# Performance work log

Measured on AMD Instinct MI355X. Metric: run time of the kernel, lower is better.

The kernel has to match this reference:

```python
import jax, jax.numpy as jnp
import numpy as np

BLANK = 0  # blank_index


def lstm_step(x, h, c, W_ih, W_hh, b_ih, b_hh):
    # torch LSTM gate order: i, f, g, o
    gates = x @ W_ih.T + h @ W_hh.T + b_ih + b_hh  # (B, 4H)
    i, f, g, o = jnp.split(gates, 4, axis=-1)
    c2 = jax.nn.sigmoid(f) * c + jax.nn.sigmoid(i) * jnp.tanh(g)
    h2 = jax.nn.sigmoid(o) * jnp.tanh(c2)
    return h2, c2


def greedy_decode(encoder_output, encoded_lengths, embedding, W_ih, W_hh, b_ih, b_hh,
                  W_enc, b_enc, W_pred, b_pred, W_out, b_out, h0, c0):
    # encoder_output: (B, H, T) -> (B, T, H), as in forward()'s transpose(1, 2)
    x = jnp.transpose(encoder_output, (0, 2, 1))
    B, T, H = x.shape

    def step(carry, inputs):
        h, c, last_label = carry          # h,c: (1,B,H); last_label: (B,) int32
        f_t, t = inputs                   # f_t: (B,H) encoder frame, t: scalar int32
        # _pred_step: SOS (zero vector) at t==0, else embed last emitted label
        emb = jnp.where(t == 0, jnp.zeros((B, H), x.dtype), embedding[last_label])
        h1, c1 = lstm_step(emb, h[0], c[0], W_ih, W_hh, b_ih, b_hh)
        # _joint_step: additive joint + relu + output proj, log_softmax (CPU path)
        joint = jax.nn.relu(f_t @ W_enc.T + b_enc + h1 @ W_pred.T + b_pred)
        logp = jax.nn.log_softmax((joint @ W_out.T + b_out).astype(jnp.float32), axis=-1)
        k = jnp.argmax(logp, axis=-1).astype(jnp.int32)  # (B,)
        # blank if past this utterance's length OR argmax is blank
        blank_mask = (t >= encoded_lengths) | (k == BLANK)
        m = blank_mask[:, None]
        # blank entries keep old RNN state and old last_label (original's gather/scatter)
        h_new = jnp.where(m, h[0], h1)[None]
        c_new = jnp.where(m, c[0], c1)[None]
        new_label = jnp.where(blank_mask, last_label, k)
        emitted = jnp.where(blank_mask, BLANK, k)  # blank == nothing emitted this step
        return (h_new, c_new, new_label), emitted

    init = (h0, c0, jnp.full((B,), BLANK, jnp.int32))
    xs = (jnp.transpose(x, (1, 0, 2)), jnp.arange(T, dtype=jnp.int32))
    (hF, cF, _), emitted = jax.lax.scan(step, init, xs)  # emitted: (T, B)
    return emitted.T, hF, cF  # labels (B,T) blank-padded, final (h, c)


def setup_inputs() -> dict:
    key = jax.random.key(0)
    ks = jax.random.split(key, 15)
    B, T, H, V1 = 128, 512, 640, 4097
    s = jnp.float32(0.1)
    return {
        "encoder_output": jax.random.normal(ks[0], (B, H, T), jnp.float32),
        "encoded_lengths": jax.random.randint(ks[1], (B,), 0, T).astype(jnp.int32),
        "embedding": jax.random.normal(ks[2], (V1, H), jnp.float32) * s,
        "W_ih": jax.random.normal(ks[3], (4 * H, H), jnp.float32) * s,
        "W_hh": jax.random.normal(ks[4], (4 * H, H), jnp.float32) * s,
        "b_ih": jax.random.normal(ks[5], (4 * H,), jnp.float32) * s,
        "b_hh": jax.random.normal(ks[6], (4 * H,), jnp.float32) * s,
        "W_enc": jax.random.normal(ks[7], (H, H), jnp.float32) * s,
        "b_enc": jax.random.normal(ks[8], (H,), jnp.float32) * s,
        "W_pred": jax.random.normal(ks[9], (H, H), jnp.float32) * s,
        "b_pred": jax.random.normal(ks[10], (H,), jnp.float32) * s,
        "W_out": jax.random.normal(ks[11], (V1, H), jnp.float32) * s,
        "b_out": jax.random.normal(ks[12], (V1,), jnp.float32) * s,
        "h0": jnp.zeros((1, B, H), jnp.float32),
        "c0": jnp.zeros((1, B, H), jnp.float32),
    }


def reference(encoder_output, encoded_lengths, embedding, W_ih, W_hh, b_ih, b_hh,
              W_enc, b_enc, W_pred, b_pred, W_out, b_out, h0, c0):
    return greedy_decode(encoder_output, encoded_lengths, embedding, W_ih, W_hh,
                         b_ih, b_hh, W_enc, b_enc, W_pred, b_pred, W_out, b_out, h0, c0)
```

## Files before the change

kernel.cpp:

```cpp
#include <hip/hip_runtime.h>
#include <stdint.h>

#define HH 640
#define BB 128
#define TT 512
#define VV 4097
#define G4 2560
#define VP3 4104
#define VE  4112

typedef float f32x4v __attribute__((ext_vector_type(4)));

__device__ __forceinline__ float sigm(float x){ return 1.0f/(1.0f+expf(-x)); }

__device__ __forceinline__ unsigned long long packkey(float f, unsigned v){
    unsigned u = __float_as_uint(f);
    unsigned m = (u & 0x80000000u) ? ~u : (u | 0x80000000u);
    return ((unsigned long long)m << 32) | (unsigned long long)(~v);
}
__device__ __forceinline__ int xcd_tile(int bid, int per){ return (bid & 7)*per + (bid >> 3); }
__device__ __forceinline__ size_t taddr(int k, int b){
    return ((size_t)(k>>2)*BB + b)*4 + (k&3);
}

__global__ __launch_bounds__(256) void k_init3(const float* __restrict__ h0, const float* __restrict__ c0,
                       float* __restrict__ hs0, float* __restrict__ csT,
                       int* __restrict__ label, unsigned long long* __restrict__ slot8){
    int i = blockIdx.x*256 + threadIdx.x;
    if (i < BB*HH){
        int b = i / HH, jj = i % HH;
        size_t o = taddr(jj, b);
        hs0[o] = h0[i]; csT[o] = c0[i];
    }
    if (i < BB) label[i] = 0;
    if (i < 8*BB) slot8[i] = 0ULL;
}

__global__ __launch_bounds__(256) void k_tr_gate(const float* __restrict__ W, float* __restrict__ WT){
    int idx = blockIdx.x*256 + threadIdx.x;
    if (idx >= G4*160) return;
    int row = idx / 160, kq = idx % 160;
    int g = row / HH, jj = row % HH;
    float4 f = *reinterpret_cast<const float4*>(W + (size_t)row*HH + kq*4);
    WT[(size_t)(kq*4+0)*G4 + jj*4+g] = f.x;
    WT[(size_t)(kq*4+1)*G4 + jj*4+g] = f.y;
    WT[(size_t)(kq*4+2)*G4 + jj*4+g] = f.z;
    WT[(size_t)(kq*4+3)*G4 + jj*4+g] = f.w;
}
__global__ __launch_bounds__(256) void k_tr640(const float* __restrict__ W, float* __restrict__ WT){
    int idx = blockIdx.x*256 + threadIdx.x;
    if (idx >= HH*160) return;
    int n = idx / 160, kq = idx % 160;
    float4 f = *reinterpret_cast<const float4*>(W + (size_t)n*HH + kq*4);
    WT[(size_t)(kq*4+0)*HH + n] = f.x;
    WT[(size_t)(kq*4+1)*HH + n] = f.y;
    WT[(size_t)(kq*4+2)*HH + n] = f.z;
    WT[(size_t)(kq*4+3)*HH + n] = f.w;
}
__global__ __launch_bounds__(256) void k_tr_wout3(const float* __restrict__ W, float* __restrict__ WT){
    int idx = blockIdx.x*256 + threadIdx.x;
    if (idx >= VP3*160) return;
    int v = idx / 160, kq = idx % 160;
    float4 f = make_float4(0.f,0.f,0.f,0.f);
    if (v < VV) f = *reinterpret_cast<const float4*>(W + (size_t)v*HH + kq*4);
    WT[(size_t)(kq*4+0)*VP3 + v] = f.x;
    WT[(size_t)(kq*4+1)*VP3 + v] = f.y;
    WT[(size_t)(kq*4+2)*VP3 + v] = f.z;
    WT[(size_t)(kq*4+3)*VP3 + v] = f.w;
}
__global__ __launch_bounds__(256) void k_boutpad3(const float* __restrict__ b_out, float* __restrict__ boutP){
    int v = blockIdx.x*256 + threadIdx.x;
    if (v < VP3) boutP[v] = (v < VV) ? b_out[v] : -1e30f;
}
__global__ __launch_bounds__(256) void k_tr_embT(const float* __restrict__ emb, float* __restrict__ embT){
    int idx = blockIdx.x*256 + threadIdx.x;
    if (idx >= 160*VE) return;
    int kq = idx / VE, v = idx % VE;
    float4 f = make_float4(0.f,0.f,0.f,0.f);
    if (v < VV) f = *reinterpret_cast<const float4*>(emb + (size_t)v*HH + kq*4);
    embT[(size_t)(kq*4+0)*VE + v] = f.x;
    embT[(size_t)(kq*4+1)*VE + v] = f.y;
    embT[(size_t)(kq*4+2)*VE + v] = f.z;
    embT[(size_t)(kq*4+3)*VE + v] = f.w;
}

__global__ __launch_bounds__(256) void k_embproj3(const float* __restrict__ embT,
                          const float* __restrict__ WihT,
                          const float* __restrict__ b_ih, const float* __restrict__ b_hh,
                          float* __restrict__ embproj){
    __shared__ float lwv[HH*16];
    int vt = blockIdx.x / 160, ut = blockIdx.x % 160;
    for (int i=threadIdx.x; i<HH*16; i+=256)
        lwv[i] = WihT[(size_t)(i>>4)*G4 + ut*16 + (i&15)];
    float bias[16];
    #pragma unroll
    for (int u=0;u<16;++u){
        int gu = ut*16+u, jj = gu>>2, g = gu&3;
        bias[u] = b_ih[g*HH+jj] + b_hh[g*HH+jj];
    }
    __syncthreads();
    int v = vt*256 + threadIdx.x;
    float acc[16];
    #pragma unroll
    for (int u=0;u<16;++u) acc[u]=0.f;
    if (v < VV){
        #pragma unroll 2
        for (int k=0;k<HH;++k){
            float e = embT[(size_t)k*VE + v];
            const f32x4v* wr = reinterpret_cast<const f32x4v*>(&lwv[k*16]);
            #pragma unroll
            for (int g=0; g<4; ++g){
                f32x4v w = wr[g];
                #pragma unroll
                for (int ee=0; ee<4; ++ee) acc[g*4+ee] = fmaf(w[ee], e, acc[g*4+ee]);
            }
        }
    }
    if (v <= VV){
        #pragma unroll
        for (int q=0;q<4;++q){
            float4 st = make_float4(acc[q*4+0]+bias[q*4+0], acc[q*4+1]+bias[q*4+1],
                                    acc[q*4+2]+bias[q*4+2], acc[q*4+3]+bias[q*4+3]);
            *reinterpret_cast<float4*>(embproj + (size_t)v*G4 + ut*16 + q*4) = st;
        }
    }
}

__global__ __launch_bounds__(128) void k_encprojT2(const float* __restrict__ x,
                          const float* __restrict__ WencT, const float* __restrict__ b_enc,
                          float* __restrict__ encprojT){
    int tile = (blockIdx.x & 7)*2560 + (blockIdx.x >> 3);
    int b   = tile / 160;
    int rem = tile % 160;
    int tt  = rem / 5;
    int nt2 = rem % 5;
    int n = nt2*128 + threadIdx.x;
    float acc[16];
    #pragma unroll
    for (int i=0;i<16;i++) acc[i]=0.f;
    const float* xb = x + (size_t)b*HH*TT + tt*16;
    #pragma unroll 4
    for (int k=0;k<HH;++k){
        float wv = WencT[(size_t)k*HH + n];
        const float4* xp = reinterpret_cast<const float4*>(xb + (size_t)k*TT);
        float4 x0=xp[0], x1=xp[1], x2=xp[2], x3=xp[3];
        acc[0]=fmaf(x0.x,wv,acc[0]);  acc[1]=fmaf(x0.y,wv,acc[1]);
        acc[2]=fmaf(x0.z,wv,acc[2]);  acc[3]=fmaf(x0.w,wv,acc[3]);
        acc[4]=fmaf(x1.x,wv,acc[4]);  acc[5]=fmaf(x1.y,wv,acc[5]);
        acc[6]=fmaf(x1.z,wv,acc[6]);  acc[7]=fmaf(x1.w,wv,acc[7]);
        acc[8]=fmaf(x2.x,wv,acc[8]);  acc[9]=fmaf(x2.y,wv,acc[9]);
        acc[10]=fmaf(x2.z,wv,acc[10]); acc[11]=fmaf(x2.w,wv,acc[11]);
        acc[12]=fmaf(x3.x,wv,acc[12]); acc[13]=fmaf(x3.y,wv,acc[13]);
        acc[14]=fmaf(x3.z,wv,acc[14]); acc[15]=fmaf(x3.w,wv,acc[15]);
    }
    float be = b_enc[n];
    #pragma unroll
    for (int ti=0; ti<16; ++ti)
        encprojT[((size_t)(tt*16+ti)*HH + n)*BB + b] = acc[ti] + be;
}


__global__ __launch_bounds__(512) void kA(
    const float* __restrict__ WhhT, const float* __restrict__ embproj,
    const int* __restrict__ lens,
    const float* __restrict__ hsrT, float* __restrict__ hswT,
    const float* __restrict__ h1rT, float* __restrict__ h1wT,
    float* __restrict__ csT, float* __restrict__ c1T,
    int* __restrict__ label, const unsigned long long* __restrict__ slot8,
    float* __restrict__ out_emit, int t)
{
    __shared__ float lw[HH*16];
    __shared__ float red[3*16*128];
    const int bid = xcd_tile(blockIdx.x, 20);
    const int tid = threadIdx.x;
    const int b = tid & 127, kh = tid >> 7;
    const int u0 = bid*16;

    for (int i=tid; i<HH*16; i+=512)
        lw[i] = WhhT[(size_t)(i>>4)*G4 + u0 + (i&15)];

    bool mask; int sel=0, kprev=0;
    if (t==0){ mask=true; sel=0; }
    else{
        unsigned long long key = slot8[b];
        #pragma unroll
        for (int q=1;q<8;++q){ unsigned long long o=slot8[q*128+b]; if(o>key)key=o; }
        int k = (int)(~(unsigned)key);
        int lab = label[b];
        mask = ((t-1) >= lens[b]) || (k==0);
        kprev = k; sel = mask ? lab : k;
    }
    __syncthreads();

    const float4* hp = reinterpret_cast<const float4*>(mask ? hsrT : h1rT);
    float a1[16];
    #pragma unroll
    for (int u=0;u<16;++u) a1[u]=0.f;
    const int k0 = kh*40;
    #pragma unroll 2
    for (int k4=k0; k4<k0+40; ++k4){
        float4 hv = hp[(size_t)k4*BB + b];
        #pragma unroll
        for (int q=0;q<4;++q){
            float h = (q==0)?hv.x:(q==1)?hv.y:(q==2)?hv.z:hv.w;
            const f32x4v* wr = reinterpret_cast<const f32x4v*>(&lw[(k4*4+q)*16]);
            #pragma unroll
            for (int g=0; g<4; ++g){
                f32x4v w = wr[g];
                #pragma unroll
                for (int ee=0; ee<4; ++ee) a1[g*4+ee] = fmaf(w[ee], h, a1[g*4+ee]);
            }
        }
    }
    if (kh > 0){
        #pragma unroll
        for (int u=0;u<16;++u) red[((kh-1)*16+u)*128 + b] = a1[u];
    }
    __syncthreads();
    if (kh == 0){
        int erow = (t==0) ? VV : sel;
        const float4* eb = reinterpret_cast<const float4*>(embproj + (size_t)erow*G4 + u0);
        const size_t g4 = (size_t)bid*BB + b;
        float4 ce4 = mask ? reinterpret_cast<const float4*>(csT)[g4]
                          : reinterpret_cast<const float4*>(c1T)[g4];
        float4 he4 = mask ? reinterpret_cast<const float4*>(hsrT)[g4]
                          : reinterpret_cast<const float4*>(h1rT)[g4];
        float cn[4], hn[4];
        const float* cep = &ce4.x;
        #pragma unroll
        for (int jl=0; jl<4; ++jl){
            float4 e = eb[jl];
            float gi = a1[jl*4+0] + red[(jl*4+0)*128+b] + red[(16+jl*4+0)*128+b] + red[(32+jl*4+0)*128+b] + e.x;
            float gf = a1[jl*4+1] + red[(jl*4+1)*128+b] + red[(16+jl*4+1)*128+b] + red[(32+jl*4+1)*128+b] + e.y;
            float gg = a1[jl*4+2] + red[(jl*4+2)*128+b] + red[(16+jl*4+2)*128+b] + red[(32+jl*4+2)*128+b] + e.z;
            float go = a1[jl*4+3] + red[(jl*4+3)*128+b] + red[(16+jl*4+3)*128+b] + red[(32+jl*4+3)*128+b] + e.w;
            float ce = cep[jl];
            float cv = sigm(gf)*ce + sigm(gi)*tanhf(gg);
            cn[jl] = cv;
            hn[jl] = sigm(go)*tanhf(cv);
        }
        reinterpret_cast<float4*>(csT)[g4]  = ce4;
        reinterpret_cast<float4*>(c1T)[g4]  = make_float4(cn[0],cn[1],cn[2],cn[3]);
        reinterpret_cast<float4*>(hswT)[g4] = he4;
        reinterpret_cast<float4*>(h1wT)[g4] = make_float4(hn[0],hn[1],hn[2],hn[3]);
        if (bid == 0){
            if (t > 0) out_emit[(size_t)b*TT + (t-1)] = mask ? 0.f : (float)kprev;
            label[b] = sel;
        }
    }
}

__global__ __launch_bounds__(512) void kB(
    const float* __restrict__ WpredT, const float* __restrict__ encprojT,
    const float* __restrict__ b_pred, const float* __restrict__ h1T,
    float* __restrict__ jointT, unsigned long long* __restrict__ slot8, int t)
{
    __shared__ float lw[HH*4];
    __shared__ float red[3*4*128];
    const int bid = xcd_tile(blockIdx.x, 20);
    const int tid = threadIdx.x;
    const int b = tid & 127, kh = tid >> 7;
    const int n0 = bid*4;
    for (int i=tid; i<HH*4; i+=512)
        lw[i] = WpredT[(size_t)(i>>2)*HH + n0 + (i&3)];
    if (bid == 0 && kh == 3){
        #pragma unroll
        for (int q=0;q<8;++q) slot8[q*128 + b] = 0ULL;
    }
    __syncthreads();
    const float4* hp = reinterpret_cast<const float4*>(h1T);
    float a[4] = {0.f,0.f,0.f,0.f};
    const int k0 = kh*40;
    #pragma unroll 2
    for (int k4=k0; k4<k0+40; ++k4){
        float4 hv = hp[(size_t)k4*BB + b];
        #pragma unroll
        for (int q=0;q<4;++q){
            float h = (q==0)?hv.x:(q==1)?hv.y:(q==2)?hv.z:hv.w;
            f32x4v w = *reinterpret_cast<const f32x4v*>(&lw[(k4*4+q)*4]);
            #pragma unroll
            for (int ee=0; ee<4; ++ee) a[ee] = fmaf(w[ee], h, a[ee]);
        }
    }
    if (kh > 0){
        #pragma unroll
        for (int u=0;u<4;++u) red[((kh-1)*4+u)*128 + b] = a[u];
    }
    __syncthreads();
    if (kh == 0){
        float jn[4];
        #pragma unroll
        for (int u=0;u<4;++u){
            float s = a[u] + red[u*128+b] + red[(4+u)*128+b] + red[(8+u)*128+b]
                    + b_pred[n0+u] + encprojT[((size_t)t*HH + n0+u)*BB + b];
            jn[u] = fmaxf(s, 0.f);
        }
        reinterpret_cast<float4*>(jointT)[(size_t)bid*BB + b] =
            make_float4(jn[0],jn[1],jn[2],jn[3]);
    }
}

__global__ __launch_bounds__(512) void kC(
    const float* __restrict__ WoutT3, const float* __restrict__ boutP3,
    const float* __restrict__ jointT, unsigned long long* __restrict__ slot8)
{
    __shared__ float lw[HH*20];
    __shared__ float red[3*19*128];
    const int bid = xcd_tile(blockIdx.x, 27);
    const int tid = threadIdx.x;
    const int b = tid & 127, kh = tid >> 7;
    const int v0 = bid*19;
    for (int i=tid; i<HH*19; i+=512){
        int k = i/19, u = i - k*19;
        lw[k*20 + u] = WoutT3[(size_t)k*VP3 + v0 + u];
    }
    __syncthreads();
    const float4* jp = reinterpret_cast<const float4*>(jointT);
    float a[19];
    #pragma unroll
    for (int u=0;u<19;++u) a[u]=0.f;
    const int k0 = kh*40;
    #pragma unroll 2
    for (int k4=k0; k4<k0+40; ++k4){
        float4 jv = jp[(size_t)k4*BB + b];
        #pragma unroll
        for (int q=0;q<4;++q){
            float h = (q==0)?jv.x:(q==1)?jv.y:(q==2)?jv.z:jv.w;
            const f32x4v* wr = reinterpret_cast<const f32x4v*>(&lw[(k4*4+q)*20]);
            #pragma unroll
            for (int g=0; g<4; ++g){
                f32x4v w = wr[g];
                #pragma unroll
                for (int ee=0; ee<4; ++ee) a[g*4+ee] = fmaf(w[ee], h, a[g*4+ee]);
            }
            f32x4v w4 = wr[4];
            a[16] = fmaf(w4[0], h, a[16]);
            a[17] = fmaf(w4[1], h, a[17]);
            a[18] = fmaf(w4[2], h, a[18]);
        }
    }
    if (kh > 0){
        #pragma unroll
        for (int u=0;u<19;++u) red[((kh-1)*19+u)*128 + b] = a[u];
    }
    __syncthreads();
    if (kh == 0){
        unsigned long long key = 0ULL;
        #pragma unroll
        for (int u=0;u<19;++u){
            float s = a[u] + red[u*128+b] + red[(19+u)*128+b] + red[(38+u)*128+b] + boutP3[v0+u];
            unsigned long long kk = packkey(s, (unsigned)(v0+u));
            if (kk > key) key = kk;
        }
        atomicMax(&slot8[(bid&7)*128 + b], key);
    }
}

__global__ __launch_bounds__(256) void kFin(const int* __restrict__ lens,
                        const unsigned long long* __restrict__ slot8,
                        const float* __restrict__ hsT, const float* __restrict__ h1T,
                        const float* __restrict__ csT, const float* __restrict__ c1T,
                        float* __restrict__ dout)
{
    int i = blockIdx.x*256 + threadIdx.x;
    if (i >= BB*HH) return;
    int b = i / HH, jj = i % HH;
    unsigned long long key = slot8[b];
    #pragma unroll
    for (int q=1;q<8;++q){ unsigned long long o=slot8[q*128+b]; if(o>key)key=o; }
    int k = (int)(~(unsigned)key);
    bool m = ((TT-1) >= lens[b]) || (k == 0);
    size_t o = taddr(jj, b);
    dout[BB*TT + i]         = m ? hsT[o] : h1T[o];
    dout[BB*TT + BB*HH + i] = m ? csT[o] : c1T[o];
    if (i < BB){
        unsigned long long key2 = slot8[i];
        #pragma unroll
        for (int q=1;q<8;++q){ unsigned long long o2=slot8[q*128+i]; if(o2>key2)key2=o2; }
        int k2 = (int)(~(unsigned)key2);
        bool mm = ((TT-1) >= lens[i]) || (k2 == 0);
        dout[(size_t)i*TT + (TT-1)] = mm ? 0.0f : (float)k2;
    }
}

__global__ __launch_bounds__(256) void k_init(const float* __restrict__ h0, const float* __restrict__ c0,
                       float* __restrict__ hs0, float* __restrict__ cs,
                       int* __restrict__ label, unsigned long long* __restrict__ slot){
    int i = blockIdx.x*256 + threadIdx.x;
    if (i < BB*HH){ hs0[i] = h0[i]; cs[i] = c0[i]; }
    if (i < BB){ label[i] = 0; slot[i] = 0ULL; }
}

__global__ __launch_bounds__(256) void k_p1o(
    const float* __restrict__ Whh, const float* __restrict__ Wih,
    const float* __restrict__ embedding,
    const float* __restrict__ b_ih, const float* __restrict__ b_hh,
    const int* __restrict__ lens,
    const float* __restrict__ hs_r, float* __restrict__ hs_w,
    const float* __restrict__ h1_r, float* __restrict__ h1_w,
    float* c_state, float* c1, int* label,
    const unsigned long long* __restrict__ slot,
    float* __restrict__ out_emit, int t)
{
    int tile = (blockIdx.x & 7)*20 + (blockIdx.x >> 3);
    int jt = tile >> 4, bg = tile & 15;
    int lane = threadIdx.x & 63, w = threadIdx.x >> 6;
    int j = (jt<<6) + lane, b0 = bg<<3;

    bool mask[8]; int kprev[8]; int sel[8];
    #pragma unroll
    for (int bi=0; bi<8; ++bi){
        int b = b0+bi;
        if (t == 0){ mask[bi]=true; sel[bi]=0; kprev[bi]=0; }
        else {
            unsigned long long key = slot[b];
            int k = (int)(~(unsigned)key);
            int lab = label[b];
            bool m = ((t-1) >= lens[b]) || (k == 0);
            mask[bi]=m; kprev[bi]=k; sel[bi] = m ? lab : k;
        }
    }
    float acc[8];
    #pragma unroll
    for (int i=0;i<8;i++) acc[i]=0.f;
    const float* wrow  = Whh + (size_t)(w*HH + j)*HH;
    const float* wrow2 = Wih + (size_t)(w*HH + j)*HH;
    for (int kc=0; kc<HH; kc+=16){
        float wv[16], wv2[16];
        #pragma unroll
        for (int q=0;q<4;q++){
            float4 f = *reinterpret_cast<const float4*>(wrow + kc + q*4);
            wv[q*4+0]=f.x; wv[q*4+1]=f.y; wv[q*4+2]=f.z; wv[q*4+3]=f.w;
            float4 f2 = *reinterpret_cast<const float4*>(wrow2 + kc + q*4);
            wv2[q*4+0]=f2.x; wv2[q*4+1]=f2.y; wv2[q*4+2]=f2.z; wv2[q*4+3]=f2.w;
        }
        #pragma unroll
        for (int bi=0; bi<8; ++bi){
            int b = b0+bi;
            const float* hp0 = hs_r + (size_t)b*HH + kc;
            const float* hp1 = h1_r + (size_t)b*HH + kc;
            float a = acc[bi];
            if (mask[bi]){
                #pragma unroll
                for (int k=0;k<16;k++) a = fmaf(hp0[k], wv[k], a);
            } else {
                #pragma unroll
                for (int k=0;k<16;k++) a = fmaf(hp1[k], wv[k], a);
            }
            if (t > 0){
                const float* ep = embedding + (size_t)sel[bi]*HH + kc;
                #pragma unroll
                for (int k=0;k<16;k++) a = fmaf(ep[k], wv2[k], a);
            }
            acc[bi] = a;
        }
    }
    __shared__ float xch[8][4][64];
    #pragma unroll
    for (int bi=0; bi<8; ++bi)
        xch[bi][w][lane] = acc[bi] + b_ih[w*HH + j] + b_hh[w*HH + j];
    __syncthreads();
    #pragma unroll
    for (int r=0; r<2; ++r){
        int bi = (w<<1) + r;
        int b  = b0 + bi;
        size_t o = (size_t)b*HH + j;
        float gi = xch[bi][0][lane], gf = xch[bi][1][lane];
        float gg = xch[bi][2][lane], go = xch[bi][3][lane];
        float ce = mask[bi] ? c_state[o] : c1[o];
        float c2 = sigm(gf)*ce + sigm(gi)*tanhf(gg);
        float h2 = sigm(go)*tanhf(c2);
        float he = mask[bi] ? hs_r[o] : h1_r[o];
        c_state[o] = ce; c1[o] = c2; hs_w[o] = he; h1_w[o] = h2;
    }
    if (jt == 0 && t > 0 && threadIdx.x < 8){
        int bi = threadIdx.x; int b = b0 + bi;
        out_emit[(size_t)b*TT + (t-1)] = mask[bi] ? 0.0f : (float)kprev[bi];
        label[b] = sel[bi];
    }
}

__global__ __launch_bounds__(128) void k_p2o(
    const float* __restrict__ Wpred, const float* __restrict__ Wenc,
    const float* __restrict__ x, const float* __restrict__ b_enc,
    const float* __restrict__ b_pred, const float* __restrict__ h1,
    float* __restrict__ joint, unsigned long long* __restrict__ slot, int t)
{
    int tile = (blockIdx.x & 7)*20 + (blockIdx.x >> 3);
    int nt = tile / 32, bg = tile % 32;
    int lane = threadIdx.x & 63, w = threadIdx.x >> 6;
    int n = nt*128 + w*64 + lane, b0 = bg*4;
    float acc[4] = {0.f,0.f,0.f,0.f};
    const float* wr  = Wpred + (size_t)n*HH;
    const float* wr2 = Wenc  + (size_t)n*HH;
    for (int kc=0; kc<HH; kc+=16){
        float wv[16], wv2[16];
        #pragma unroll
        for (int q=0;q<4;q++){
            float4 f = *reinterpret_cast<const float4*>(wr + kc + q*4);
            wv[q*4+0]=f.x; wv[q*4+1]=f.y; wv[q*4+2]=f.z; wv[q*4+3]=f.w;
            float4 f2 = *reinterpret_cast<const float4*>(wr2 + kc + q*4);
            wv2[q*4+0]=f2.x; wv2[q*4+1]=f2.y; wv2[q*4+2]=f2.z; wv2[q*4+3]=f2.w;
        }
        #pragma unroll
        for (int bi=0; bi<4; ++bi){
            int b = b0+bi;
            const float* hp = h1 + (size_t)b*HH + kc;
            float a = acc[bi];
            #pragma unroll
            for (int k=0;k<16;k++) a = fmaf(hp[k], wv[k], a);
            const float* xp = x + (size_t)b*HH*TT + (size_t)kc*TT + t;
            #pragma unroll
            for (int k=0;k<16;k++) a = fmaf(xp[(size_t)k*TT], wv2[k], a);
            acc[bi] = a;
        }
    }
    #pragma unroll
    for (int bi=0; bi<4; ++bi){
        int b = b0+bi;
        joint[(size_t)b*HH + n] = fmaxf(acc[bi] + b_pred[n] + b_enc[n], 0.0f);
    }
    if (tile == 0) slot[threadIdx.x] = 0ULL;
}

__global__ __launch_bounds__(256) void k_p3o(
    const float* __restrict__ Wout, const float* __restrict__ b_out,
    const float* __restrict__ joint, unsigned long long* __restrict__ slot)
{
    int tile = (blockIdx.x & 7)*34 + (blockIdx.x >> 3);
    int vt = tile >> 4, bg = tile & 15;
    int lane = threadIdx.x & 63, w = threadIdx.x >> 6;
    int v = vt*256 + w*64 + lane;
    bool valid = v < VV;
    int vv = valid ? v : (VV-1);
    int b0 = bg*8;
    float acc[8];
    #pragma unroll
    for (int i=0;i<8;i++) acc[i]=0.f;
    const float* wr = Wout + (size_t)vv*HH;
    for (int kc=0; kc<HH; kc+=16){
        float wv[16];
        #pragma unroll
        for (int q=0;q<4;q++){
            float4 f = *reinterpret_cast<const float4*>(wr + kc + q*4);
            wv[q*4+0]=f.x; wv[q*4+1]=f.y; wv[q*4+2]=f.z; wv[q*4+3]=f.w;
        }
        #pragma unroll
        for (int bi=0; bi<8; ++bi){
            int b = b0+bi;
            const float* jp = joint + (size_t)b*HH + kc;
            float a = acc[bi];
            #pragma unroll
            for (int k=0;k<16;k++) a = fmaf(jp[k], wv[k], a);
            acc[bi] = a;
        }
    }
    float bofl = b_out[vv];
    __shared__ unsigned long long redo[4][8];
    #pragma unroll
    for (int bi=0; bi<8; ++bi){
        unsigned long long key = valid ? packkey(acc[bi] + bofl, (unsigned)v) : 0ULL;
        #pragma unroll
        for (int off=32; off>0; off>>=1){
            unsigned long long o = __shfl_xor(key, off, 64);
            if (o > key) key = o;
        }
        if (lane == 0) redo[w][bi] = key;
    }
    __syncthreads();
    if (threadIdx.x < 8){
        int bi = threadIdx.x;
        unsigned long long m = redo[0][bi];
        #pragma unroll
        for (int q=1;q<4;q++) if (redo[q][bi] > m) m = redo[q][bi];
        atomicMax(&slot[b0+bi], m);
    }
}

__global__ __launch_bounds__(256) void k_finalo(const int* __restrict__ lens,
                        const unsigned long long* __restrict__ slot,
                        const float* __restrict__ hs_r, const float* __restrict__ h1_r,
                        const float* __restrict__ cs,  const float* __restrict__ c1,
                        float* __restrict__ dout)
{
    int i = blockIdx.x*256 + threadIdx.x;
    if (i >= BB*HH) return;
    int b = i / HH;
    unsigned long long key = slot[b];
    int k = (int)(~(unsigned)key);
    bool m = ((TT-1) >= lens[b]) || (k == 0);
    dout[BB*TT + i]         = m ? hs_r[i] : h1_r[i];
    dout[BB*TT + BB*HH + i] = m ? cs[i]   : c1[i];
    if (i < BB){
        unsigned long long key2 = slot[i];
        int k2 = (int)(~(unsigned)key2);
        bool mm = ((TT-1) >= lens[i]) || (k2 == 0);
        dout[(size_t)i*TT + (TT-1)] = mm ? 0.0f : (float)k2;
    }
}

extern "C" void kernel_launch(void* const* d_in, const int* in_sizes, int n_in,
                              void* d_out, int out_size, void* d_ws, size_t ws_size,
                              hipStream_t stream)
{
    const float* x     = (const float*)d_in[0];
    const int*   lens  = (const int*)  d_in[1];
    const float* emb   = (const float*)d_in[2];
    const float* Wih   = (const float*)d_in[3];
    const float* Whh   = (const float*)d_in[4];
    const float* bih   = (const float*)d_in[5];
    const float* bhh   = (const float*)d_in[6];
    const float* Wenc  = (const float*)d_in[7];
    const float* benc  = (const float*)d_in[8];
    const float* Wpred = (const float*)d_in[9];
    const float* bpred = (const float*)d_in[10];
    const float* Wout  = (const float*)d_in[11];
    const float* bout  = (const float*)d_in[12];
    const float* h0    = (const float*)d_in[13];
    const float* c0    = (const float*)d_in[14];
    float* out = (float*)d_out;
    (void)in_sizes; (void)n_in; (void)out_size;

    char* ws = (char*)d_ws;
    size_t off = 0;
    auto alloc = [&](size_t bytes) -> void* {
        void* p = ws + off; off += (bytes + 255) & ~(size_t)255; return p;
    };
    auto aligned = [](size_t bytes){ return (bytes + 255) & ~(size_t)255; };

    const size_t BH = (size_t)BB*HH*sizeof(float);
    float* hs0  = (float*)alloc(BH);
    float* hs1  = (float*)alloc(BH);
    float* h1b0 = (float*)alloc(BH);
    float* h1b1 = (float*)alloc(BH);
    float* cs   = (float*)alloc(BH);
    float* c1   = (float*)alloc(BH);
    float* joint= (float*)alloc(BH);
    int* label  = (int*)alloc(BB*sizeof(int));
    unsigned long long* slot8 = (unsigned long long*)alloc(8*BB*sizeof(unsigned long long));

    size_t need = off
        + aligned((size_t)HH*G4*sizeof(float))
        + aligned((size_t)HH*G4*sizeof(float))
        + aligned((size_t)HH*HH*sizeof(float))
        + aligned((size_t)HH*HH*sizeof(float))
        + aligned((size_t)HH*VP3*sizeof(float))
        + aligned((size_t)VP3*sizeof(float))
        + aligned((size_t)HH*VE*sizeof(float))
        + aligned((size_t)(VV+1)*G4*sizeof(float))
        + aligned((size_t)TT*BB*HH*sizeof(float));

    if (ws_size >= need){
        float* WhhT   = (float*)alloc((size_t)HH*G4*sizeof(float));
        float* WihT   = (float*)alloc((size_t)HH*G4*sizeof(float));
        float* WpredT = (float*)alloc((size_t)HH*HH*sizeof(float));
        float* WencT  = (float*)alloc((size_t)HH*HH*sizeof(float));
        float* WoutT3 = (float*)alloc((size_t)HH*VP3*sizeof(float));
        float* boutP3 = (float*)alloc((size_t)VP3*sizeof(float));
        float* embT   = (float*)alloc((size_t)HH*VE*sizeof(float));
        float* embproj= (float*)alloc((size_t)(VV+1)*G4*sizeof(float));
        float* encprojT=(float*)alloc((size_t)TT*BB*HH*sizeof(float));

        k_init3<<<(BB*HH+255)/256, 256, 0, stream>>>(h0, c0, hs0, cs, label, slot8);
        k_tr_gate<<<(G4*160+255)/256, 256, 0, stream>>>(Whh, WhhT);
        k_tr_gate<<<(G4*160+255)/256, 256, 0, stream>>>(Wih, WihT);
        k_tr640 <<<(HH*160+255)/256, 256, 0, stream>>>(Wpred, WpredT);
        k_tr640 <<<(HH*160+255)/256, 256, 0, stream>>>(Wenc,  WencT);
        k_tr_wout3<<<(VP3*160+255)/256, 256, 0, stream>>>(Wout, WoutT3);
        k_boutpad3<<<(VP3+255)/256, 256, 0, stream>>>(bout, boutP3);
        k_tr_embT<<<(160*VE+255)/256, 256, 0, stream>>>(emb, embT);
        k_embproj3<<<17*160, 256, 0, stream>>>(embT, WihT, bih, bhh, embproj);
        k_encprojT2<<<20480, 128, 0, stream>>>(x, WencT, benc, encprojT);

        float* hsbuf[2] = {hs0, hs1};
        float* h1buf[2] = {h1b0, h1b1};
        for (int t = 0; t < TT; ++t){
            const float* hsr = hsbuf[t & 1];
            float*       hsw = hsbuf[(t+1) & 1];
            const float* h1r = h1buf[(t+1) & 1];
            float*       h1w = h1buf[t & 1];
            kA<<<160, 512, 0, stream>>>(WhhT, embproj, lens, hsr, hsw, h1r, h1w,
                                        cs, c1, label, slot8, out, t);
            kB<<<160, 512, 0, stream>>>(WpredT, encprojT, bpred, h1w, joint, slot8, t);
            kC<<<216, 512, 0, stream>>>(WoutT3, boutP3, joint, slot8);
        }
        kFin<<<(BB*HH+255)/256, 256, 0, stream>>>(lens, slot8, hsbuf[0], h1buf[1], cs, c1, out);
        return;
    }

    unsigned long long* slot = slot8;
    k_init<<<(BB*HH+255)/256, 256, 0, stream>>>(h0, c0, hs0, cs, label, slot);
    float* hsbuf[2] = {hs0, hs1};
    float* h1buf[2] = {h1b0, h1b1};
    for (int t = 0; t < TT; ++t){
        const float* hsr = hsbuf[t & 1];
        float*       hsw = hsbuf[(t+1) & 1];
        const float* h1r = h1buf[(t+1) & 1];
        float*       h1w = h1buf[t & 1];
        k_p1o<<<160, 256, 0, stream>>>(Whh, Wih, emb, bih, bhh, lens,
                                       hsr, hsw, h1r, h1w, cs, c1, label, slot, out, t);
        k_p2o<<<160, 128, 0, stream>>>(Wpred, Wenc, x, benc, bpred, h1w, joint, slot, t);
        k_p3o<<<272, 256, 0, stream>>>(Wout, bout, joint, slot);
    }
    k_finalo<<<(BB*HH+255)/256, 256, 0, stream>>>(lens, slot, hsbuf[0], h1buf[1], cs, c1, out);
}
```

Baseline: 33.09 ms.

## Replace per-step kernel launches with persistent cooperative kernel using per-XCD barriers

Replaces the three kernel launches per timestep (1536 launches in total) with a single persistent cooperative kernel of 256 blocks. Each XCD owns 16 batch rows and synchronises through atomic spin barriers in global memory. The kernel also fuses the W_hh and W_pred matvecs into one concatenated weight matrix, computing the gate pre-activations for the next step together with the joint projection, and uses new k4-interleaved weight layouts. The aim is to remove launch overhead and inter-kernel gaps. The cost is reliance on co-residency, hardware XCD id reads, volatile memory traffic and spin-wait timeouts, which adds correctness and deadlock risk.

```diff
diff --git a/kernel.cpp b/kernel.cpp
--- a/kernel.cpp
+++ b/kernel.cpp
@@ -6,8 +6,11 @@
 #define TT 512
 #define VV 4097
 #define G4 2560
-#define VP3 4104
-#define VE  4112
+#define VE 4112
+#define XS 10240
+#define XG 40960
+#define NC2 3200
+#define NC3 4096
 
 typedef float f32x4v __attribute__((ext_vector_type(4)));
 
@@ -18,22 +21,26 @@
     unsigned m = (u & 0x80000000u) ? ~u : (u | 0x80000000u);
     return ((unsigned long long)m << 32) | (unsigned long long)(~v);
 }
-__device__ __forceinline__ int xcd_tile(int bid, int per){ return (bid & 7)*per + (bid >> 3); }
-__device__ __forceinline__ size_t taddr(int k, int b){
-    return ((size_t)(k>>2)*BB + b)*4 + (k&3);
-}
-
-__global__ __launch_bounds__(256) void k_init3(const float* __restrict__ h0, const float* __restrict__ c0,
-                       float* __restrict__ hs0, float* __restrict__ csT,
-                       int* __restrict__ label, unsigned long long* __restrict__ slot8){
+
+__device__ __forceinline__ float vld(const float* p){ return *(const volatile float*)p; }
+__device__ __forceinline__ void  vst(float* p, float v){ *(volatile float*)p = v; }
+__device__ __forceinline__ int   vldi(const int* p){ return *(const volatile int*)p; }
+__device__ __forceinline__ void  vsti(int* p, int v){ *(volatile int*)p = v; }
+
+__global__ __launch_bounds__(256) void k_init4(const float* __restrict__ h0, const float* __restrict__ c0,
+                       float* __restrict__ hcm, float* __restrict__ cs,
+                       int* __restrict__ labelP, unsigned long long* __restrict__ slot,
+                       int* __restrict__ ctrl){
     int i = blockIdx.x*256 + threadIdx.x;
     if (i < BB*HH){
         int b = i / HH, jj = i % HH;
-        size_t o = taddr(jj, b);
-        hs0[o] = h0[i]; csT[o] = c0[i];
-    }
-    if (i < BB) label[i] = 0;
-    if (i < 8*BB) slot8[i] = 0ULL;
+        int x = b >> 4, bl = b & 15;
+        size_t o = (size_t)x*XS + jj*16 + bl;
+        hcm[o] = h0[i]; cs[o] = c0[i];
+    }
+    if (i < BB) slot[i] = 0ULL;
+    if (i < 8*32) labelP[i] = 0;
+    if (i < 2048) ctrl[i] = 0;
 }
 
 __global__ __launch_bounds__(256) void k_tr_gate(const float* __restrict__ W, float* __restrict__ WT){
@@ -57,21 +64,6 @@
     WT[(size_t)(kq*4+2)*HH + n] = f.z;
     WT[(size_t)(kq*4+3)*HH + n] = f.w;
 }
-__global__ __launch_bounds__(256) void k_tr_wout3(const float* __restrict__ W, float* __restrict__ WT){
-    int idx = blockIdx.x*256 + threadIdx.x;
-    if (idx >= VP3*160) return;
-    int v = idx / 160, kq = idx % 160;
-    float4 f = make_float4(0.f,0.f,0.f,0.f);
-    if (v < VV) f = *reinterpret_cast<const float4*>(W + (size_t)v*HH + kq*4);
-    WT[(size_t)(kq*4+0)*VP3 + v] = f.x;
-    WT[(size_t)(kq*4+1)*VP3 + v] = f.y;
-    WT[(size_t)(kq*4+2)*VP3 + v] = f.z;
-    WT[(size_t)(kq*4+3)*VP3 + v] = f.w;
-}
-__global__ __launch_bounds__(256) void k_boutpad3(const float* __restrict__ b_out, float* __restrict__ boutP){
-    int v = blockIdx.x*256 + threadIdx.x;
-    if (v < VP3) boutP[v] = (v < VV) ? b_out[v] : -1e30f;
-}
 __global__ __launch_bounds__(256) void k_tr_embT(const float* __restrict__ emb, float* __restrict__ embT){
     int idx = blockIdx.x*256 + threadIdx.x;
     if (idx >= 160*VE) return;
@@ -82,6 +74,30 @@
     embT[(size_t)(kq*4+1)*VE + v] = f.y;
     embT[(size_t)(kq*4+2)*VE + v] = f.z;
     embT[(size_t)(kq*4+3)*VE + v] = f.w;
+}
+__global__ __launch_bounds__(256) void k_tr_WJ(const float* __restrict__ Whh, const float* __restrict__ Wpred,
+                        float* __restrict__ WJ){
+    int idx = blockIdx.x*256 + threadIdx.x;
+    if (idx >= NC2*160) return;
+    int u = idx / 160, k4 = idx % 160;
+    float4 f;
+    if (u < G4){
+        int jj = u >> 2, g = u & 3;
+        f = *reinterpret_cast<const float4*>(Whh + (size_t)(g*HH+jj)*HH + k4*4);
+    } else {
+        int n = u - G4;
+        f = *reinterpret_cast<const float4*>(Wpred + (size_t)n*HH + k4*4);
+    }
+    float* d = WJ + ((size_t)k4*NC2 + u)*4;
+    d[0]=f.x; d[1]=f.y; d[2]=f.z; d[3]=f.w;
+}
+__global__ __launch_bounds__(256) void k_tr_woutk4(const float* __restrict__ Wout, float* __restrict__ WK){
+    int idx = blockIdx.x*256 + threadIdx.x;
+    if (idx >= NC3*160) return;
+    int v = idx / 160, k4 = idx % 160;
+    float4 f = *reinterpret_cast<const float4*>(Wout + (size_t)v*HH + k4*4);
+    float* d = WK + ((size_t)k4*NC3 + v)*4;
+    d[0]=f.x; d[1]=f.y; d[2]=f.z; d[3]=f.w;
 }
 
 __global__ __launch_bounds__(256) void k_embproj3(const float* __restrict__ embT,
@@ -159,224 +175,280 @@
         encprojT[((size_t)(tt*16+ti)*HH + n)*BB + b] = acc[ti] + be;
 }
 
-
-__global__ __launch_bounds__(512) void kA(
-    const float* __restrict__ WhhT, const float* __restrict__ embproj,
-    const int* __restrict__ lens,
-    const float* __restrict__ hsrT, float* __restrict__ hswT,
-    const float* __restrict__ h1rT, float* __restrict__ h1wT,
-    float* __restrict__ csT, float* __restrict__ c1T,
-    int* __restrict__ label, const unsigned long long* __restrict__ slot8,
-    float* __restrict__ out_emit, int t)
+__global__ __launch_bounds__(512) void k_gcm0(const float* __restrict__ WJ, const float* __restrict__ h0,
+                       float* __restrict__ gcm){
+    __shared__ float stage[XS];
+    __shared__ float red[3*128*16];
+    int x = blockIdx.x / 20, rr = blockIdx.x % 20;
+    int tid = threadIdx.x;
+    for (int i=tid; i<XS; i+=512)
+        stage[i] = h0[(size_t)(x*16 + (i&15))*HH + (i>>4)];
+    __syncthreads();
+    const int lane = tid & 127, kq = tid >> 7;
+    const int u = rr*128 + lane;
+    float acc[16];
+    #pragma unroll
+    for (int j=0;j<16;++j) acc[j]=0.f;
+    const float4* wp = reinterpret_cast<const float4*>(WJ) + (size_t)(kq*40)*NC2 + u;
+    for (int it=0; it<40; ++it){
+        float4 wj = *wp; wp += NC2;
+        const int kb = (kq*40 + it)*4;
+        #pragma unroll
+        for (int ks=0; ks<4; ++ks){
+            float wk = (ks==0)?wj.x:(ks==1)?wj.y:(ks==2)?wj.z:wj.w;
+            const float4* hp4 = reinterpret_cast<const float4*>(&stage[(kb+ks)*16]);
+            float4 h0v=hp4[0], h1v=hp4[1], h2v=hp4[2], h3v=hp4[3];
+            acc[0]=fmaf(wk,h0v.x,acc[0]);  acc[1]=fmaf(wk,h0v.y,acc[1]);
+            acc[2]=fmaf(wk,h0v.z,acc[2]);  acc[3]=fmaf(wk,h0v.w,acc[3]);
+            acc[4]=fmaf(wk,h1v.x,acc[4]);  acc[5]=fmaf(wk,h1v.y,acc[5]);
+            acc[6]=fmaf(wk,h1v.z,acc[6]);  acc[7]=fmaf(wk,h1v.w,acc[7]);
+            acc[8]=fmaf(wk,h2v.x,acc[8]);  acc[9]=fmaf(wk,h2v.y,acc[9]);
+            acc[10]=fmaf(wk,h2v.z,acc[10]); acc[11]=fmaf(wk,h2v.w,acc[11]);
+            acc[12]=fmaf(wk,h3v.x,acc[12]); acc[13]=fmaf(wk,h3v.y,acc[13]);
+            acc[14]=fmaf(wk,h3v.z,acc[14]); acc[15]=fmaf(wk,h3v.w,acc[15]);
+        }
+    }
+    if (kq > 0){
+        #pragma unroll
+        for (int j=0;j<16;++j) red[(kq-1)*2048 + lane*16 + j] = acc[j];
+    }
+    __syncthreads();
+    if (kq == 0){
+        #pragma unroll
+        for (int j=0;j<16;++j) acc[j] += red[lane*16+j] + red[2048+lane*16+j] + red[4096+lane*16+j];
+        int jj = u >> 2, g = u & 3;
+        #pragma unroll
+        for (int bl=0; bl<16; ++bl)
+            gcm[(size_t)x*XG + (jj*16+bl)*4 + g] = acc[bl];
+    }
+}
+
+__global__ __launch_bounds__(512,1) void k_run(
+    const float* __restrict__ WJ, const float* __restrict__ WoutK4,
+    const float* __restrict__ WoutRaw, const float* __restrict__ b_pred,
+    const float* __restrict__ b_out, const float* __restrict__ embproj,
+    const float* __restrict__ encprojT, const int* __restrict__ lens,
+    float* hcm, float* h1s, float* cs, float* c1,
+    float* gcm, float* gnew, float* jointA,
+    unsigned long long* slot, int* labelP, int* ctrl,
+    float* dout, int guard)
 {
-    __shared__ float lw[HH*16];
-    __shared__ float red[3*16*128];
-    const int bid = xcd_tile(blockIdx.x, 20);
+    __shared__ float stage[XS];
+    __shared__ float red[3*128*16];
+    __shared__ unsigned long long keys[128*16];
+    __shared__ float padf[2048];
     const int tid = threadIdx.x;
-    const int b = tid & 127, kh = tid >> 7;
-    const int u0 = bid*16;
-
-    for (int i=tid; i<HH*16; i+=512)
-        lw[i] = WhhT[(size_t)(i>>4)*G4 + u0 + (i&15)];
-
-    bool mask; int sel=0, kprev=0;
-    if (t==0){ mask=true; sel=0; }
-    else{
-        unsigned long long key = slot8[b];
-        #pragma unroll
-        for (int q=1;q<8;++q){ unsigned long long o=slot8[q*128+b]; if(o>key)key=o; }
-        int k = (int)(~(unsigned)key);
-        int lab = label[b];
-        mask = ((t-1) >= lens[b]) || (k==0);
-        kprev = k; sel = mask ? lab : k;
+    if (guard){ padf[tid & 2047] = (float)guard; stage[0] += padf[1]; }
+
+    int xcd = __builtin_amdgcn_s_getreg(63508) & 7;
+
+    __shared__ int s_r, s_R;
+    if (tid == 0){
+        s_r = (int)__hip_atomic_fetch_add((unsigned*)&ctrl[xcd], 1u, __ATOMIC_RELAXED, __HIP_MEMORY_SCOPE_AGENT);
+        __hip_atomic_fetch_add((unsigned*)&ctrl[16], 1u, __ATOMIC_RELAXED, __HIP_MEMORY_SCOPE_AGENT);
+        long spin = 0;
+        while (__hip_atomic_load((unsigned*)&ctrl[16], __ATOMIC_RELAXED, __HIP_MEMORY_SCOPE_AGENT) < 256u
+               && spin < 400000000L){ __builtin_amdgcn_s_sleep(1); ++spin; }
+        s_R = (int)__hip_atomic_load((unsigned*)&ctrl[xcd], __ATOMIC_RELAXED, __HIP_MEMORY_SCOPE_AGENT);
     }
     __syncthreads();
-
-    const float4* hp = reinterpret_cast<const float4*>(mask ? hsrT : h1rT);
-    float a1[16];
-    #pragma unroll
-    for (int u=0;u<16;++u) a1[u]=0.f;
-    const int k0 = kh*40;
-    #pragma unroll 2
-    for (int k4=k0; k4<k0+40; ++k4){
-        float4 hv = hp[(size_t)k4*BB + b];
-        #pragma unroll
-        for (int q=0;q<4;++q){
-            float h = (q==0)?hv.x:(q==1)?hv.y:(q==2)?hv.z:hv.w;
-            const f32x4v* wr = reinterpret_cast<const f32x4v*>(&lw[(k4*4+q)*16]);
+    const int r = s_r;
+    const int R = s_R;
+    unsigned* bcp = (unsigned*)&ctrl[32 + xcd*32];
+    const int b0 = xcd*16;
+
+    float* hcmX = hcm + (size_t)xcd*XS;
+    float* h1X  = h1s + (size_t)xcd*XS;
+    float* csX  = cs  + (size_t)xcd*XS;
+    float* c1X  = c1  + (size_t)xcd*XS;
+    float* gcmX = gcm + (size_t)xcd*XG;
+    float* gnewX= gnew+ (size_t)xcd*XG;
+    float* jX   = jointA + (size_t)xcd*XS;
+    int* labX   = labelP + xcd*32;
+
+    unsigned ph = 0;
+    #define LBAR() do { \
+        asm volatile("s_waitcnt vmcnt(0) lgkmcnt(0)" ::: "memory"); \
+        __syncthreads(); \
+        ++ph; \
+        if (tid == 0){ \
+            __hip_atomic_fetch_add(bcp, 1u, __ATOMIC_RELAXED, __HIP_MEMORY_SCOPE_AGENT); \
+            long spin = 0; unsigned tgt = ph * (unsigned)R; \
+            while (__hip_atomic_load(bcp, __ATOMIC_RELAXED, __HIP_MEMORY_SCOPE_AGENT) < tgt \
+                   && spin < 400000000L){ __builtin_amdgcn_s_sleep(1); ++spin; } \
+        } \
+        __syncthreads(); \
+        asm volatile("" ::: "memory"); \
+    } while(0)
+
+    for (int t = 0; t < TT; ++t){
+        for (int u = r*512 + tid; u < XS; u += R*512){
+            int jj = u >> 4, bl = u & 15, b = b0 + bl;
+            bool mask; int sel = 0, kprev = 0;
+            if (t == 0){ mask = true; sel = 0; }
+            else {
+                unsigned long long key = __hip_atomic_load(&slot[b], __ATOMIC_RELAXED, __HIP_MEMORY_SCOPE_AGENT);
+                int k = (int)(~(unsigned)key);
+                int lab = vldi(labX + bl);
+                mask = ((t-1) >= lens[b]) || (k == 0);
+                kprev = k; sel = mask ? lab : k;
+            }
+            size_t go = (size_t)u*4;
+            const float* gs = (mask ? gcmX : gnewX) + go;
+            float ghx = vld(gs+0), ghy = vld(gs+1), ghz = vld(gs+2), ghw = vld(gs+3);
+            if (!mask){ float* gd = gcmX + go; vst(gd+0,ghx); vst(gd+1,ghy); vst(gd+2,ghz); vst(gd+3,ghw); }
+            int erow = (t == 0) ? VV : sel;
+            float4 e = reinterpret_cast<const float4*>(embproj)[(size_t)erow*640 + jj];
+            float gi = ghx+e.x, gf = ghy+e.y, gg = ghz+e.z, goo = ghw+e.w;
+            float ce = mask ? vld(csX+u) : vld(c1X+u);
+            float cv = sigm(gf)*ce + sigm(gi)*tanhf(gg);
+            float h2 = sigm(goo)*tanhf(cv);
+            float he = mask ? vld(hcmX+u) : vld(h1X+u);
+            vst(csX+u, ce); vst(c1X+u, cv); vst(hcmX+u, he); vst(h1X+u, h2);
+            if (jj == 0){
+                if (t > 0) dout[(size_t)b*TT + (t-1)] = mask ? 0.f : (float)kprev;
+                vsti(labX + bl, sel);
+            }
+        }
+        LBAR();
+
+        for (int i = tid; i < XS; i += 512) stage[i] = vld(h1X + i);
+        if (r == R-1 && tid < 16)
+            __hip_atomic_store(&slot[b0+tid], 0ULL, __ATOMIC_RELAXED, __HIP_MEMORY_SCOPE_AGENT);
+        __syncthreads();
+        for (int w = r; w < 25; w += R){
+            const int lane = tid & 127, kq = tid >> 7;
+            const int u = w*128 + lane;
+            float acc[16];
             #pragma unroll
-            for (int g=0; g<4; ++g){
-                f32x4v w = wr[g];
-                #pragma unroll
-                for (int ee=0; ee<4; ++ee) a1[g*4+ee] = fmaf(w[ee], h, a1[g*4+ee]);
-            }
-        }
-    }
-    if (kh > 0){
-        #pragma unroll
-        for (int u=0;u<16;++u) red[((kh-1)*16+u)*128 + b] = a1[u];
-    }
-    __syncthreads();
-    if (kh == 0){
-        int erow = (t==0) ? VV : sel;
-        const float4* eb = reinterpret_cast<const float4*>(embproj + (size_t)erow*G4 + u0);
-        const size_t g4 = (size_t)bid*BB + b;
-        float4 ce4 = mask ? reinterpret_cast<const float4*>(csT)[g4]
-                          : reinterpret_cast<const float4*>(c1T)[g4];
-        float4 he4 = mask ? reinterpret_cast<const float4*>(hsrT)[g4]
-                          : reinterpret_cast<const float4*>(h1rT)[g4];
-        float cn[4], hn[4];
-        const float* cep = &ce4.x;
-        #pragma unroll
-        for (int jl=0; jl<4; ++jl){
-            float4 e = eb[jl];
-            float gi = a1[jl*4+0] + red[(jl*4+0)*128+b] + red[(16+jl*4+0)*128+b] + red[(32+jl*4+0)*128+b] + e.x;
-            float gf = a1[jl*4+1] + red[(jl*4+1)*128+b] + red[(16+jl*4+1)*128+b] + red[(32+jl*4+1)*128+b] + e.y;
-            float gg = a1[jl*4+2] + red[(jl*4+2)*128+b] + red[(16+jl*4+2)*128+b] + red[(32+jl*4+2)*128+b] + e.z;
-            float go = a1[jl*4+3] + red[(jl*4+3)*128+b] + red[(16+jl*4+3)*128+b] + red[(32+jl*4+3)*128+b] + e.w;
-            float ce = cep[jl];
-            float cv = sigm(gf)*ce + sigm(gi)*tanhf(gg);
-            cn[jl] = cv;
-            hn[jl] = sigm(go)*tanhf(cv);
-        }
-        reinterpret_cast<float4*>(csT)[g4]  = ce4;
-        reinterpret_cast<float4*>(c1T)[g4]  = make_float4(cn[0],cn[1],cn[2],cn[3]);
-        reinterpret_cast<float4*>(hswT)[g4] = he4;
-        reinterpret_cast<float4*>(h1wT)[g4] = make_float4(hn[0],hn[1],hn[2],hn[3]);
-        if (bid == 0){
-            if (t > 0) out_emit[(size_t)b*TT + (t-1)] = mask ? 0.f : (float)kprev;
-            label[b] = sel;
-        }
-    }
-}
-
-__global__ __launch_bounds__(512) void kB(
-    const float* __restrict__ WpredT, const float* __restrict__ encprojT,
-    const float* __restrict__ b_pred, const float* __restrict__ h1T,
-    float* __restrict__ jointT, unsigned long long* __restrict__ slot8, int t)
-{
-    __shared__ float lw[HH*4];
-    __shared__ float red[3*4*128];
-    const int bid = xcd_tile(blockIdx.x, 20);
-    const int tid = threadIdx.x;
-    const int b = tid & 127, kh = tid >> 7;
-    const int n0 = bid*4;
-    for (int i=tid; i<HH*4; i+=512)
-        lw[i] = WpredT[(size_t)(i>>2)*HH + n0 + (i&3)];
-    if (bid == 0 && kh == 3){
-        #pragma unroll
-        for (int q=0;q<8;++q) slot8[q*128 + b] = 0ULL;
-    }
-    __syncthreads();
-    const float4* hp = reinterpret_cast<const float4*>(h1T);
-    float a[4] = {0.f,0.f,0.f,0.f};
-    const int k0 = kh*40;
-    #pragma unroll 2
-    for (int k4=k0; k4<k0+40; ++k4){
-        float4 hv = hp[(size_t)k4*BB + b];
-        #pragma unroll
-        for (int q=0;q<4;++q){
-            float h = (q==0)?hv.x:(q==1)?hv.y:(q==2)?hv.z:hv.w;
-            f32x4v w = *reinterpret_cast<const f32x4v*>(&lw[(k4*4+q)*4]);
+            for (int j=0;j<16;++j) acc[j]=0.f;
+            const float4* wp = reinterpret_cast<const float4*>(WJ) + (size_t)(kq*40)*NC2 + u;
+            for (int it=0; it<40; ++it){
+                float4 wj = *wp; wp += NC2;
+                const int kb = (kq*40 + it)*4;
+                #pragma unroll
+                for (int ks=0; ks<4; ++ks){
+                    float wk = (ks==0)?wj.x:(ks==1)?wj.y:(ks==2)?wj.z:wj.w;
+                    const float4* hp4 = reinterpret_cast<const float4*>(&stage[(kb+ks)*16]);
+                    float4 h0v=hp4[0], h1v=hp4[1], h2v=hp4[2], h3v=hp4[3];
+                    acc[0]=fmaf(wk,h0v.x,acc[0]);  acc[1]=fmaf(wk,h0v.y,acc[1]);
+                    acc[2]=fmaf(wk,h0v.z,acc[2]);  acc[3]=fmaf(wk,h0v.w,acc[3]);
+                    acc[4]=fmaf(wk,h1v.x,acc[4]);  acc[5]=fmaf(wk,h1v.y,acc[5]);
+                    acc[6]=fmaf(wk,h1v.z,acc[6]);  acc[7]=fmaf(wk,h1v.w,acc[7]);
+                    acc[8]=fmaf(wk,h2v.x,acc[8]);  acc[9]=fmaf(wk,h2v.y,acc[9]);
+                    acc[10]=fmaf(wk,h2v.z,acc[10]); acc[11]=fmaf(wk,h2v.w,acc[11]);
+                    acc[12]=fmaf(wk,h3v.x,acc[12]); acc[13]=fmaf(wk,h3v.y,acc[13]);
+                    acc[14]=fmaf(wk,h3v.z,acc[14]); acc[15]=fmaf(wk,h3v.w,acc[15]);
+                }
+            }
+            if (kq > 0){
+                #pragma unroll
+                for (int j=0;j<16;++j) red[(kq-1)*2048 + lane*16 + j] = acc[j];
+            }
+            __syncthreads();
+            if (kq == 0){
+                #pragma unroll
+                for (int j=0;j<16;++j) acc[j] += red[lane*16+j] + red[2048+lane*16+j] + red[4096+lane*16+j];
+                if (u < G4){
+                    int jj = u >> 2, g = u & 3;
+                    #pragma unroll
+                    for (int bl=0; bl<16; ++bl) vst(gnewX + (size_t)(jj*16+bl)*4 + g, acc[bl]);
+                } else {
+                    int n = u - G4;
+                    float bp = b_pred[n];
+                    const float* ep = encprojT + ((size_t)t*HH + n)*BB + b0;
+                    #pragma unroll
+                    for (int bl=0; bl<16; ++bl){
+                        float s = acc[bl] + bp + ep[bl];
+                        vst(jX + n*16 + bl, fmaxf(s, 0.f));
+                    }
+                }
+            }
+            __syncthreads();
+        }
+        LBAR();
+
+        for (int i = tid; i < XS; i += 512) stage[i] = vld(jX + i);
+        __syncthreads();
+        for (int w = r; w < 32; w += R){
+            const int lane = tid & 127, kq = tid >> 7;
+            const int v = w*128 + lane;
+            float acc[16];
             #pragma unroll
-            for (int ee=0; ee<4; ++ee) a[ee] = fmaf(w[ee], h, a[ee]);
-        }
-    }
-    if (kh > 0){
-        #pragma unroll
-        for (int u=0;u<4;++u) red[((kh-1)*4+u)*128 + b] = a[u];
-    }
-    __syncthreads();
-    if (kh == 0){
-        float jn[4];
-        #pragma unroll
-        for (int u=0;u<4;++u){
-            float s = a[u] + red[u*128+b] + red[(4+u)*128+b] + red[(8+u)*128+b]
-                    + b_pred[n0+u] + encprojT[((size_t)t*HH + n0+u)*BB + b];
-            jn[u] = fmaxf(s, 0.f);
-        }
-        reinterpret_cast<float4*>(jointT)[(size_t)bid*BB + b] =
-            make_float4(jn[0],jn[1],jn[2],jn[3]);
-    }
-}
-
-__global__ __launch_bounds__(512) void kC(
-    const float* __restrict__ WoutT3, const float* __restrict__ boutP3,
-    const float* __restrict__ jointT, unsigned long long* __restrict__ slot8)
-{
-    __shared__ float lw[HH*20];
-    __shared__ float red[3*19*128];
-    const int bid = xcd_tile(blockIdx.x, 27);
-    const int tid = threadIdx.x;
-    const int b = tid & 127, kh = tid >> 7;
-    const int v0 = bid*19;
-    for (int i=tid; i<HH*19; i+=512){
-        int k = i/19, u = i - k*19;
-        lw[k*20 + u] = WoutT3[(size_t)k*VP3 + v0 + u];
-    }
-    __syncthreads();
-    const float4* jp = reinterpret_cast<const float4*>(jointT);
-    float a[19];
-    #pragma unroll
-    for (int u=0;u<19;++u) a[u]=0.f;
-    const int k0 = kh*40;
-    #pragma unroll 2
-    for (int k4=k0; k4<k0+40; ++k4){
-        float4 jv = jp[(size_t)k4*BB + b];
-        #pragma unroll
-        for (int q=0;q<4;++q){
-            float h = (q==0)?jv.x:(q==1)?jv.y:(q==2)?jv.z:jv.w;
-            const f32x4v* wr = reinterpret_cast<const f32x4v*>(&lw[(k4*4+q)*20]);
-            #pragma unroll
-            for (int g=0; g<4; ++g){
-                f32x4v w = wr[g];
-                #pragma unroll
-                for (int ee=0; ee<4; ++ee) a[g*4+ee] = fmaf(w[ee], h, a[g*4+ee]);
-            }
-            f32x4v w4 = wr[4];
-            a[16] = fmaf(w4[0], h, a[16]);
-            a[17] = fmaf(w4[1], h, a[17]);
-            a[18] = fmaf(w4[2], h, a[18]);
-        }
-    }
-    if (kh > 0){
-        #pragma unroll
-        for (int u=0;u<19;++u) red[((kh-1)*19+u)*128 + b] = a[u];
-    }
-    __syncthreads();
-    if (kh == 0){
-        unsigned long long key = 0ULL;
-        #pragma unroll
-        for (int u=0;u<19;++u){
-            float s = a[u] + red[u*128+b] + red[(19+u)*128+b] + red[(38+u)*128+b] + boutP3[v0+u];
-            unsigned long long kk = packkey(s, (unsigned)(v0+u));
-            if (kk > key) key = kk;
-        }
-        atomicMax(&slot8[(bid&7)*128 + b], key);
-    }
-}
-
-__global__ __launch_bounds__(256) void kFin(const int* __restrict__ lens,
-                        const unsigned long long* __restrict__ slot8,
-                        const float* __restrict__ hsT, const float* __restrict__ h1T,
-                        const float* __restrict__ csT, const float* __restrict__ c1T,
+            for (int j=0;j<16;++j) acc[j]=0.f;
+            const float4* wp = reinterpret_cast<const float4*>(WoutK4) + (size_t)(kq*40)*NC3 + v;
+            for (int it=0; it<40; ++it){
+                float4 wj = *wp; wp += NC3;
+                const int kb = (kq*40 + it)*4;
+                #pragma unroll
+                for (int ks=0; ks<4; ++ks){
+                    float wk = (ks==0)?wj.x:(ks==1)?wj.y:(ks==2)?wj.z:wj.w;
+                    const float4* hp4 = reinterpret_cast<const float4*>(&stage[(kb+ks)*16]);
+                    float4 h0v=hp4[0], h1v=hp4[1], h2v=hp4[2], h3v=hp4[3];
+                    acc[0]=fmaf(wk,h0v.x,acc[0]);  acc[1]=fmaf(wk,h0v.y,acc[1]);
+                    acc[2]=fmaf(wk,h0v.z,acc[2]);  acc[3]=fmaf(wk,h0v.w,acc[3]);
+                    acc[4]=fmaf(wk,h1v.x,acc[4]);  acc[5]=fmaf(wk,h1v.y,acc[5]);
+                    acc[6]=fmaf(wk,h1v.z,acc[6]);  acc[7]=fmaf(wk,h1v.w,acc[7]);
+                    acc[8]=fmaf(wk,h2v.x,acc[8]);  acc[9]=fmaf(wk,h2v.y,acc[9]);
+                    acc[10]=fmaf(wk,h2v.z,acc[10]); acc[11]=fmaf(wk,h2v.w,acc[11]);
+                    acc[12]=fmaf(wk,h3v.x,acc[12]); acc[13]=fmaf(wk,h3v.y,acc[13]);
+                    acc[14]=fmaf(wk,h3v.z,acc[14]); acc[15]=fmaf(wk,h3v.w,acc[15]);
+                }
+            }
+            if (kq > 0){
+                #pragma unroll
+                for (int j=0;j<16;++j) red[(kq-1)*2048 + lane*16 + j] = acc[j];
+            }
+            __syncthreads();
+            if (kq == 0){
+                float bo = b_out[v];
+                #pragma unroll
+                for (int bl=0; bl<16; ++bl){
+                    float s = acc[bl] + red[lane*16+bl] + red[2048+lane*16+bl] + red[4096+lane*16+bl] + bo;
+                    keys[lane*16+bl] = packkey(s, (unsigned)v);
+                }
+            }
+            __syncthreads();
+            if (tid < 16){
+                unsigned long long best = 0ULL;
+                for (int l=0; l<128; ++l){
+                    unsigned long long kk = keys[l*16+tid];
+                    if (kk > best) best = kk;
+                }
+                __hip_atomic_fetch_max(&slot[b0+tid], best, __ATOMIC_RELAXED, __HIP_MEMORY_SCOPE_AGENT);
+            }
+            __syncthreads();
+        }
+        if (r == R-1 && tid < 16){
+            float a = 0.f;
+            const float* wr = WoutRaw + (size_t)4096*HH;
+            for (int k=0; k<HH; ++k) a = fmaf(wr[k], stage[k*16+tid], a);
+            unsigned long long kk = packkey(a + b_out[4096], 4096u);
+            __hip_atomic_fetch_max(&slot[b0+tid], kk, __ATOMIC_RELAXED, __HIP_MEMORY_SCOPE_AGENT);
+        }
+        LBAR();
+    }
+    #undef LBAR
+}
+
+__global__ __launch_bounds__(256) void kFin2(const int* __restrict__ lens,
+                        const unsigned long long* __restrict__ slot,
+                        const float* __restrict__ hcm, const float* __restrict__ h1s,
+                        const float* __restrict__ cs,  const float* __restrict__ c1,
                         float* __restrict__ dout)
 {
     int i = blockIdx.x*256 + threadIdx.x;
     if (i >= BB*HH) return;
     int b = i / HH, jj = i % HH;
-    unsigned long long key = slot8[b];
-    #pragma unroll
-    for (int q=1;q<8;++q){ unsigned long long o=slot8[q*128+b]; if(o>key)key=o; }
+    int x = b >> 4, bl = b & 15;
+    size_t o = (size_t)x*XS + jj*16 + bl;
+    unsigned long long key = slot[b];
     int k = (int)(~(unsigned)key);
     bool m = ((TT-1) >= lens[b]) || (k == 0);
-    size_t o = taddr(jj, b);
-    dout[BB*TT + i]         = m ? hsT[o] : h1T[o];
-    dout[BB*TT + BB*HH + i] = m ? csT[o] : c1T[o];
+    dout[BB*TT + i]         = m ? hcm[o] : h1s[o];
+    dout[BB*TT + BB*HH + i] = m ? cs[o]  : c1[o];
     if (i < BB){
-        unsigned long long key2 = slot8[i];
-        #pragma unroll
-        for (int q=1;q<8;++q){ unsigned long long o2=slot8[q*128+i]; if(o2>key2)key2=o2; }
+        unsigned long long key2 = slot[i];
         int k2 = (int)(~(unsigned)key2);
         bool mm = ((TT-1) >= lens[i]) || (k2 == 0);
         dout[(size_t)i*TT + (TT-1)] = mm ? 0.0f : (float)k2;
@@ -384,10 +456,10 @@
 }
 
 __global__ __launch_bounds__(256) void k_init(const float* __restrict__ h0, const float* __restrict__ c0,
-                       float* __restrict__ hs0, float* __restrict__ cs,
+                       float* __restrict__ hs0, float* __restrict__ cso,
                        int* __restrict__ label, unsigned long long* __restrict__ slot){
     int i = blockIdx.x*256 + threadIdx.x;
-    if (i < BB*HH){ hs0[i] = h0[i]; cs[i] = c0[i]; }
+    if (i < BB*HH){ hs0[i] = h0[i]; cso[i] = c0[i]; }
     if (i < BB){ label[i] = 0; slot[i] = 0ULL; }
 }
 
@@ -398,7 +470,7 @@
     const int* __restrict__ lens,
     const float* __restrict__ hs_r, float* __restrict__ hs_w,
     const float* __restrict__ h1_r, float* __restrict__ h1_w,
-    float* c_state, float* c1, int* label,
+    float* c_state, float* c1o, int* label,
     const unsigned long long* __restrict__ slot,
     float* __restrict__ out_emit, int t)
 {
@@ -461,17 +533,17 @@
         xch[bi][w][lane] = acc[bi] + b_ih[w*HH + j] + b_hh[w*HH + j];
     __syncthreads();
     #pragma unroll
-    for (int r=0; r<2; ++r){
-        int bi = (w<<1) + r;
+    for (int rr=0; rr<2; ++rr){
+        int bi = (w<<1) + rr;
         int b  = b0 + bi;
         size_t o = (size_t)b*HH + j;
         float gi = xch[bi][0][lane], gf = xch[bi][1][lane];
         float gg = xch[bi][2][lane], go = xch[bi][3][lane];
-        float ce = mask[bi] ? c_state[o] : c1[o];
+        float ce = mask[bi] ? c_state[o] : c1o[o];
         float c2 = sigm(gf)*ce + sigm(gi)*tanhf(gg);
         float h2 = sigm(go)*tanhf(c2);
         float he = mask[bi] ? hs_r[o] : h1_r[o];
-        c_state[o] = ce; c1[o] = c2; hs_w[o] = he; h1_w[o] = h2;
+        c_state[o] = ce; c1o[o] = c2; hs_w[o] = he; h1_w[o] = h2;
     }
     if (jt == 0 && t > 0 && threadIdx.x < 8){
         int bi = threadIdx.x; int b = b0 + bi;
@@ -580,7 +652,7 @@
 __global__ __launch_bounds__(256) void k_finalo(const int* __restrict__ lens,
                         const unsigned long long* __restrict__ slot,
                         const float* __restrict__ hs_r, const float* __restrict__ h1_r,
-                        const float* __restrict__ cs,  const float* __restrict__ c1,
+                        const float* __restrict__ cso,  const float* __restrict__ c1o,
                         float* __restrict__ dout)
 {
     int i = blockIdx.x*256 + threadIdx.x;
@@ -590,7 +662,7 @@
     int k = (int)(~(unsigned)key);
     bool m = ((TT-1) >= lens[b]) || (k == 0);
     dout[BB*TT + i]         = m ? hs_r[i] : h1_r[i];
-    dout[BB*TT + BB*HH + i] = m ? cs[i]   : c1[i];
+    dout[BB*TT + BB*HH + i] = m ? cso[i]  : c1o[i];
     if (i < BB){
         unsigned long long key2 = slot[i];
         int k2 = (int)(~(unsigned)key2);
@@ -626,52 +698,71 @@
     auto alloc = [&](size_t bytes) -> void* {
         void* p = ws + off; off += (bytes + 255) & ~(size_t)255; return p;
     };
-    auto aligned = [](size_t bytes){ return (bytes + 255) & ~(size_t)255; };
-
-    const size_t BH = (size_t)BB*HH*sizeof(float);
-    float* hs0  = (float*)alloc(BH);
-    float* hs1  = (float*)alloc(BH);
-    float* h1b0 = (float*)alloc(BH);
-    float* h1b1 = (float*)alloc(BH);
-    float* cs   = (float*)alloc(BH);
-    float* c1   = (float*)alloc(BH);
-    float* joint= (float*)alloc(BH);
-    int* label  = (int*)alloc(BB*sizeof(int));
-    unsigned long long* slot8 = (unsigned long long*)alloc(8*BB*sizeof(unsigned long long));
-
-    size_t need = off
-        + aligned((size_t)HH*G4*sizeof(float))
-        + aligned((size_t)HH*G4*sizeof(float))
-        + aligned((size_t)HH*HH*sizeof(float))
-        + aligned((size_t)HH*HH*sizeof(float))
-        + aligned((size_t)HH*VP3*sizeof(float))
-        + aligned((size_t)VP3*sizeof(float))
-        + aligned((size_t)HH*VE*sizeof(float))
-        + aligned((size_t)(VV+1)*G4*sizeof(float))
-        + aligned((size_t)TT*BB*HH*sizeof(float));
-
-    if (ws_size >= need){
-        float* WhhT   = (float*)alloc((size_t)HH*G4*sizeof(float));
-        float* WihT   = (float*)alloc((size_t)HH*G4*sizeof(float));
-        float* WpredT = (float*)alloc((size_t)HH*HH*sizeof(float));
-        float* WencT  = (float*)alloc((size_t)HH*HH*sizeof(float));
-        float* WoutT3 = (float*)alloc((size_t)HH*VP3*sizeof(float));
-        float* boutP3 = (float*)alloc((size_t)VP3*sizeof(float));
-        float* embT   = (float*)alloc((size_t)HH*VE*sizeof(float));
-        float* embproj= (float*)alloc((size_t)(VV+1)*G4*sizeof(float));
-        float* encprojT=(float*)alloc((size_t)TT*BB*HH*sizeof(float));
-
-        k_init3<<<(BB*HH+255)/256, 256, 0, stream>>>(h0, c0, hs0, cs, label, slot8);
-        k_tr_gate<<<(G4*160+255)/256, 256, 0, stream>>>(Whh, WhhT);
+
+    float* hcm   = (float*)alloc(8*XS*sizeof(float));
+    float* h1s   = (float*)alloc(8*XS*sizeof(float));
+    float* cs    = (float*)alloc(8*XS*sizeof(float));
+    float* c1    = (float*)alloc(8*XS*sizeof(float));
+    float* gcm   = (float*)alloc(8*XG*sizeof(float));
+    float* gnew  = (float*)alloc(8*XG*sizeof(float));
+    float* jointA= (float*)alloc(8*XS*sizeof(float));
+    unsigned long long* slot = (unsigned long long*)alloc(BB*sizeof(unsigned long long));
+    int* labelP  = (int*)alloc(8*32*sizeof(int));
+    int* ctrl    = (int*)alloc(2048*sizeof(int));
+    char* Rbig   = (char*)alloc(19001344);
+    float* embproj = (float*)alloc((size_t)(VV+1)*G4*sizeof(float));
+    float* encprojT= (float*)alloc((size_t)TT*BB*HH*sizeof(float));
+    size_t needNew = off;
+
+    if (ws_size >= needNew){
+        float* WihT  = (float*)(Rbig);
+        float* embT  = (float*)(Rbig + 6553600);
+        float* WencT = (float*)(Rbig + 17080320);
+        float* WJ     = (float*)(Rbig);
+        float* WoutK4 = (float*)(Rbig + 8192000);
+
+        k_init4<<<(BB*HH+255)/256, 256, 0, stream>>>(h0, c0, hcm, cs, labelP, slot, ctrl);
         k_tr_gate<<<(G4*160+255)/256, 256, 0, stream>>>(Wih, WihT);
-        k_tr640 <<<(HH*160+255)/256, 256, 0, stream>>>(Wpred, WpredT);
-        k_tr640 <<<(HH*160+255)/256, 256, 0, stream>>>(Wenc,  WencT);
-        k_tr_wout3<<<(VP3*160+255)/256, 256, 0, stream>>>(Wout, WoutT3);
-        k_boutpad3<<<(VP3+255)/256, 256, 0, stream>>>(bout, boutP3);
         k_tr_embT<<<(160*VE+255)/256, 256, 0, stream>>>(emb, embT);
+        k_tr640 <<<(HH*160+255)/256, 256, 0, stream>>>(Wenc, WencT);
         k_embproj3<<<17*160, 256, 0, stream>>>(embT, WihT, bih, bhh, embproj);
         k_encprojT2<<<20480, 128, 0, stream>>>(x, WencT, benc, encprojT);
-
+        k_tr_WJ<<<(NC2*160+255)/256, 256, 0, stream>>>(Whh, Wpred, WJ);
+        k_tr_woutk4<<<(NC3*160+255)/256, 256, 0, stream>>>(Wout, WoutK4);
+        k_gcm0<<<160, 512, 0, stream>>>(WJ, h0, gcm);
+
+        const float* a0 = WJ;      const float* a1 = WoutK4;
+        const float* a2 = Wout;    const float* a3 = bpred;
+        const float* a4 = bout;    const float* a5 = embproj;
+        const float* a6 = encprojT; const int*  a7 = lens;
+        float* a8 = hcm;  float* a9 = h1s;  float* a10 = cs;  float* a11 = c1;
+        float* a12 = gcm; float* a13 = gnew; float* a14 = jointA;
+        unsigned long long* a15 = slot; int* a16 = labelP; int* a17 = ctrl;
+        float* a18 = out; int a19 = 0;
+        void* args[] = {&a0,&a1,&a2,&a3,&a4,&a5,&a6,&a7,&a8,&a9,&a10,&a11,
+                        &a12,&a13,&a14,&a15,&a16,&a17,&a18,&a19};
+        hipLaunchCooperativeKernel((const void*)k_run, dim3(256), dim3(512), args, 0, stream);
+        kFin2<<<(BB*HH+255)/256, 256, 0, stream>>>(lens, slot, hcm, h1s, cs, c1, out);
+        return;
+    }
+
+    {
+        size_t foff = 0;
+        auto falloc = [&](size_t bytes) -> void* {
+            void* p = ws + foff; foff += (bytes + 255) & ~(size_t)255; return p;
+        };
+        const size_t BH = (size_t)BB*HH*sizeof(float);
+        float* hs0  = (float*)falloc(BH);
+        float* hs1  = (float*)falloc(BH);
+        float* h1b0 = (float*)falloc(BH);
+        float* h1b1 = (float*)falloc(BH);
+        float* cso  = (float*)falloc(BH);
+        float* c1o  = (float*)falloc(BH);
+        float* joint= (float*)falloc(BH);
+        int* label  = (int*)falloc(BB*sizeof(int));
+        unsigned long long* slotf = (unsigned long long*)falloc(BB*sizeof(unsigned long long));
+
+        k_init<<<(BB*HH+255)/256, 256, 0, stream>>>(h0, c0, hs0, cso, label, slotf);
         float* hsbuf[2] = {hs0, hs1};
         float* h1buf[2] = {h1b0, h1b1};
         for (int t = 0; t < TT; ++t){
@@ -679,28 +770,11 @@
             float*       hsw = hsbuf[(t+1) & 1];
             const float* h1r = h1buf[(t+1) & 1];
             float*       h1w = h1buf[t & 1];
-            kA<<<160, 512, 0, stream>>>(WhhT, embproj, lens, hsr, hsw, h1r, h1w,
-                                        cs, c1, label, slot8, out, t);
-            kB<<<160, 512, 0, stream>>>(WpredT, encprojT, bpred, h1w, joint, slot8, t);
-            kC<<<216, 512, 0, stream>>>(WoutT3, boutP3, joint, slot8);
-        }
-        kFin<<<(BB*HH+255)/256, 256, 0, stream>>>(lens, slot8, hsbuf[0], h1buf[1], cs, c1, out);
-        return;
-    }
-
-    unsigned long long* slot = slot8;
-    k_init<<<(BB*HH+255)/256, 256, 0, stream>>>(h0, c0, hs0, cs, label, slot);
-    float* hsbuf[2] = {hs0, hs1};
-    float* h1buf[2] = {h1b0, h1b1};
-    for (int t = 0; t < TT; ++t){
-        const float* hsr = hsbuf[t & 1];
-        float*       hsw = hsbuf[(t+1) & 1];
-        const float* h1r = h1buf[(t+1) & 1];
-        float*       h1w = h1buf[t & 1];
-        k_p1o<<<160, 256, 0, stream>>>(Whh, Wih, emb, bih, bhh, lens,
-                                       hsr, hsw, h1r, h1w, cs, c1, label, slot, out, t);
-        k_p2o<<<160, 128, 0, stream>>>(Wpred, Wenc, x, benc, bpred, h1w, joint, slot, t);
-        k_p3o<<<272, 256, 0, stream>>>(Wout, bout, joint, slot);
-    }
-    k_finalo<<<(BB*HH+255)/256, 256, 0, stream>>>(lens, slot, hsbuf[0], h1buf[1], cs, c1, out);
-}
+            k_p1o<<<160, 256, 0, stream>>>(Whh, Wih, emb, bih, bhh, lens,
+                                           hsr, hsw, h1r, h1w, cso, c1o, label, slotf, out, t);
+            k_p2o<<<160, 128, 0, stream>>>(Wpred, Wenc, x, benc, bpred, h1w, joint, slotf, t);
+            k_p3o<<<272, 256, 0, stream>>>(Wout, bout, joint, slotf);
+        }
+        k_finalo<<<(BB*HH+255)/256, 256, 0, stream>>>(lens, slotf, hsbuf[0], h1buf[1], cso, c1o, out);
+    }
+}
```

Result: slower. 37.00 ms (+11.8%).
